# Optimization experiments

Hardware: AMD Instinct MI355X
Metric: run time of the kernel (lower is better)

## Reference

```python
import jax, jax.numpy as jnp
import numpy as np

B, T, S, D = 32, 1024, 1024, 512
VOCAB = 1000
INSERT_TOK = jnp.array([1, 2], dtype=jnp.int64)


def setup_inputs() -> dict:
    key = jax.random.key(0)
    k1, k2, k3, k4, k5 = jax.random.split(key, 5)
    input_var = jax.random.randint(k1, (B, T), 0, VOCAB, dtype=jnp.int64)
    output = jax.random.normal(k2, (B, T, D), jnp.float32)
    context = jax.random.normal(k3, (B, S, D), jnp.float32)
    # nn.Linear(2*dim, dim): weight [D, 2D], bias [D]
    W = jax.random.normal(k4, (D, 2 * D), jnp.float32) / np.sqrt(2 * D)
    b = jax.random.normal(k5, (D,), jnp.float32) * 0.01
    return {"input_var": input_var, "output": output, "context": context,
            "di": 0, "W": W, "b": b}


def _hard_align(input_var, src_len):
    """Replicates the python double-loop: sequential 'inserted' counter per batch.
    Returns (j, valid): j[b,i] = column of the 1.0 in attn row i (torch negative
    indices wrapped), valid[b,i] = whether row i gets any 1.0 at all."""
    bsz, tgt_len = input_var.shape
    flags = jnp.isin(input_var, INSERT_TOK)  # [B,T] is token an insert token

    def step(inserted, xi):
        i, flag = xi  # i: scalar position, flag: [B]
        cond = (src_len >= i - inserted)                    # gate, per batch
        ins2 = inserted + jnp.where(cond & flag, 1, 0)      # increment before write
        j = i - ins2 - 1
        j = jnp.where(j < 0, j + src_len, j)                # torch negative-index wrap
        return ins2, (j, cond)

    idxs = jnp.arange(1, tgt_len, dtype=jnp.int32)
    init = jnp.zeros((bsz,), jnp.int32)  # init_inserted()
    _, (j_rows, valid) = jax.lax.scan(step, init, (idxs, flags[:, 1:].T))
    j_rows = j_rows.T      # [B,T-1]
    valid = valid.T        # [B,T-1]
    # row 0: attn[b,0,0] = 1.0 always
    j_full = jnp.concatenate([jnp.zeros((bsz, 1), j_rows.dtype), j_rows], axis=1)
    valid_full = jnp.concatenate([jnp.ones((bsz, 1), bool), valid], axis=1)
    return j_full, valid_full


def reference(input_var, output, context, di, W, b):
    bsz, tgt_len, hid = output.shape
    src_len = context.shape[1]
    j, valid = _hard_align(input_var, src_len)              # [B,T], [B,T]
    vf = valid[:, :, None].astype(output.dtype)
    # hard one-hot attention matrix (as the module materializes it)
    attn = jax.nn.one_hot(j, src_len, dtype=output.dtype) * vf  # [B,T,S]
    # mix = bmm(attn, context) == masked gather of context rows
    mix = jnp.take_along_axis(context, j[:, :, None].astype(jnp.int32), axis=1) * vf
    combined = jnp.concatenate([mix, output], axis=-1)      # [B,T,2D]
    out = jnp.tanh(combined @ W.T + b)                      # [B,T,D]
    return out, attn
```

## Files before the change

### kernel.cpp

```cpp
#include <hip/hip_runtime.h>
#include <hip/hip_bf16.h>

#define B_ 32
#define T_ 1024
#define S_ 1024
#define D_ 512
#define M_ (B_*T_)
#define N_ D_
#define K_ (2*D_)

typedef __attribute__((ext_vector_type(8))) short bf16x8;
typedef __attribute__((ext_vector_type(4))) float f32x4;

__device__ inline unsigned short f2bf(float x) {
    union { float f; unsigned u; } v; v.f = x;
    unsigned r = v.u + 0x7FFFu + ((v.u >> 16) & 1u);
    return (unsigned short)(r >> 16);
}

__device__ inline unsigned cvt2bf(float lo, float hi) {
#if __has_builtin(__builtin_amdgcn_cvt_pk_bf16_f32)
    typedef __attribute__((ext_vector_type(2))) __bf16 bf2;
    union { bf2 v; unsigned u; } r;
    r.v = __builtin_amdgcn_cvt_pk_bf16_f32(lo, hi);
    return r.u;
#else
    return (unsigned)f2bf(lo) | ((unsigned)f2bf(hi) << 16);
#endif
}

__device__ inline float fast_tanh(float x) {
#if __has_builtin(__builtin_amdgcn_exp2f) && __has_builtin(__builtin_amdgcn_rcpf)
    const float e = __builtin_amdgcn_exp2f(x * 2.885390082f);
    const float r = __builtin_amdgcn_rcpf(e + 1.0f);
    return 1.0f - 2.0f * r;
#else
    return tanhf(x);
#endif
}

__global__ void align_kernel(const int* __restrict__ iv, int* __restrict__ jbuf) {
    const int b = blockIdx.x;
    const int lane = threadIdx.x;
    const int* row = iv + b * T_;
    int f[16];
    int local = 0;
    const int t0 = lane * 16;
    #pragma unroll
    for (int q = 0; q < 16; ++q) {
        const int t = t0 + q;
        const int tok = row[t];
        const int fl = (t > 0 && (tok == 1 || tok == 2)) ? 1 : 0;
        f[q] = fl;
        local += fl;
    }
    int incl = local;
    #pragma unroll
    for (int off = 1; off < 64; off <<= 1) {
        const int up = __shfl_up(incl, off, 64);
        if (lane >= off) incl += up;
    }
    int run = incl - local;
    #pragma unroll
    for (int q = 0; q < 16; ++q) {
        const int t = t0 + q;
        run += f[q];
        int j;
        if (t == 0) {
            j = 0;
        } else {
            j = t - run - 1;
            if (j < 0) j += S_;
        }
        jbuf[b * T_ + t] = j;
    }
}

__global__ void pack_w(const float* __restrict__ W, unsigned short* __restrict__ Wbf) {
    const int idx = blockIdx.x * blockDim.x + threadIdx.x;
    const f32x4 a = ((const f32x4*)W)[idx * 2];
    const f32x4 c = ((const f32x4*)W)[idx * 2 + 1];
    union { bf16x8 v; unsigned u[4]; } pk;
    pk.u[0] = cvt2bf(a[0], a[1]); pk.u[1] = cvt2bf(a[2], a[3]);
    pk.u[2] = cvt2bf(c[0], c[1]); pk.u[3] = cvt2bf(c[2], c[3]);
    *(bf16x8*)(Wbf + (size_t)idx * 8) = pk.v;
}

#define BM 256
#define BN 256
#define BK 64
#define NIT (K_ / BK)
#define KMAX (K_ - BK)
#define NGEMM ((M_ / BM) * (N_ / BN))

__global__ __launch_bounds__(512, 2)
void gemm_attn(const unsigned short* __restrict__ Wbf,
               const float* __restrict__ bias,
               float* __restrict__ out,
               float* __restrict__ attn,
               const float* __restrict__ ctx,
               const float* __restrict__ outp,
               const int* __restrict__ jbuf) {
    const int bx = blockIdx.x;
    const int tid = threadIdx.x;

    __shared__ unsigned short As[BM * BK];
    __shared__ unsigned short Bs[BN * BK];

    const int lane = tid & 63;
    const int wave = tid >> 6;
    const int wm = wave >> 1, wn = wave & 1;
    const int l16 = lane & 15, quad = lane >> 4;

    const int xcd = bx & 7;
    const int bn  = (bx >> 3) & 1;
    const int bm  = ((bx >> 4) << 3) | xcd;
    const int mBase = bm * BM;
    const int nBase = bn * BN;

    const int g    = tid & 7;
    const int rsub = tid >> 3;
    const int sw   = g ^ (rsub & 7);
    const float* actx[4];
    const float* aout[4];
    const unsigned short* bSrc[4];
    #pragma unroll
    for (int it = 0; it < 4; ++it) {
        const int r = it * 64 + rsub;
        const int m = mBase + r;
        const int jm = jbuf[m];
        actx[it] = ctx + ((size_t)((m >> 10) * S_ + jm)) * D_ + g * 8;
        aout[it] = outp + (size_t)m * D_ - D_ + g * 8;
        bSrc[it] = Wbf + (size_t)(nBase + r) * K_ + sw * 8;
    }

    const int aBase = mBase + bn * 128;

    f32x4 acc[4][8] = {};
    f32x4 fa[4][2];

#define LOAD_A(KO) do {                                                        \
    const int _koa = (KO);                                                     \
    _Pragma("unroll")                                                          \
    for (int _it = 0; _it < 4; ++_it) {                                        \
        const float* _src = (_koa < D_) ? (actx[_it] + _koa) : (aout[_it] + _koa); \
        fa[_it][0] = ((const f32x4*)_src)[0];                                  \
        fa[_it][1] = ((const f32x4*)_src)[1];                                  \
    }                                                                          \
} while (0)

    LOAD_A(0);

    #pragma unroll 1
    for (int i = 0; i < NIT; ++i) {
        const int ko = i * BK;
        #pragma unroll
        for (int it = 0; it < 4; ++it) {
            __builtin_amdgcn_global_load_lds(
                (const __attribute__((address_space(1))) void*)(bSrc[it] + ko),
                (__attribute__((address_space(3))) void*)(Bs + (it * 512 + tid) * 8),
                16, 0, 0);
        }
        #pragma unroll
        for (int it = 0; it < 4; ++it) {
            union { bf16x8 v; unsigned u[4]; } pk;
            pk.u[0] = cvt2bf(fa[it][0][0], fa[it][0][1]);
            pk.u[1] = cvt2bf(fa[it][0][2], fa[it][0][3]);
            pk.u[2] = cvt2bf(fa[it][1][0], fa[it][1][1]);
            pk.u[3] = cvt2bf(fa[it][1][2], fa[it][1][3]);
            *(bf16x8*)&As[(it * 512 + rsub * 8 + sw) * 8] = pk.v;
        }
        __syncthreads();

        {
            const int arow = aBase + i * 8 + wave;
            const int jv = jbuf[arow];
            f32x4* abase = (f32x4*)(attn + (size_t)arow * S_);
            #pragma unroll
            for (int s = 0; s < 4; ++s) {
                const int col = lane + 64 * s;
                f32x4 v = {0.f, 0.f, 0.f, 0.f};
                if ((jv >> 2) == col) v[jv & 3] = 1.0f;
                __builtin_nontemporal_store(v, abase + col);
            }
        }

        {
            const int ko2 = (ko + BK > KMAX) ? KMAX : ko + BK;
            LOAD_A(ko2);
        }

        #pragma unroll
        for (int ks = 0; ks < 2; ++ks) {
            bf16x8 af[4], bfr[8];
            const int q = ks * 4 + quad;
            #pragma unroll
            for (int mt = 0; mt < 4; ++mt) {
                const int r = wm * 64 + mt * 16 + l16;
                af[mt] = *(const bf16x8*)&As[(r * 8 + (q ^ (r & 7))) * 8];
            }
            #pragma unroll
            for (int nt = 0; nt < 8; ++nt) {
                const int rb = wn * 128 + nt * 16 + l16;
                bfr[nt] = *(const bf16x8*)&Bs[(rb * 8 + (q ^ (rb & 7))) * 8];
            }
            #pragma unroll
            for (int mt = 0; mt < 4; ++mt)
                #pragma unroll
                for (int nt = 0; nt < 8; ++nt)
                    acc[mt][nt] = __builtin_amdgcn_mfma_f32_16x16x32_bf16(
                        af[mt], bfr[nt], acc[mt][nt], 0, 0, 0);
        }
        __syncthreads();
    }

#undef LOAD_A

    #pragma unroll
    for (int nt = 0; nt < 8; ++nt) {
        const int n = nBase + wn * 128 + nt * 16 + l16;
        const float bv = bias[n];
        #pragma unroll
        for (int mt = 0; mt < 4; ++mt) {
            #pragma unroll
            for (int r = 0; r < 4; ++r) {
                const int m = mBase + wm * 64 + mt * 16 + quad * 4 + r;
                const float val = fast_tanh(acc[mt][nt][r] + bv);
                __builtin_nontemporal_store(val, &out[(size_t)m * N_ + n]);
            }
        }
    }
}

extern "C" void kernel_launch(void* const* d_in, const int* in_sizes, int n_in,
                              void* d_out, int out_size, void* d_ws, size_t ws_size,
                              hipStream_t stream) {
    const int*   iv   = (const int*)d_in[0];
    const float* outp = (const float*)d_in[1];
    const float* ctx  = (const float*)d_in[2];
    const float* W    = (const float*)d_in[4];
    const float* bias = (const float*)d_in[5];

    float* out  = (float*)d_out;
    float* attn = out + (size_t)M_ * N_;

    int* jbuf = (int*)d_ws;
    unsigned short* Wbf = (unsigned short*)((char*)d_ws + (size_t)M_ * 4);

    align_kernel<<<B_, 64, 0, stream>>>(iv, jbuf);
    pack_w<<<(N_ * K_ / 8) / 256, 256, 0, stream>>>(W, Wbf);
    gemm_attn<<<NGEMM, 512, 0, stream>>>(Wbf, bias, out, attn, ctx, outp, jbuf);
}
```

Baseline: 322.9 us.

## Double-buffer W tiles in LDS and fuse align and pack kernels

Splits the LDS buffer for the B (weight) tile into two halves. The DMA for the next K step is issued into the spare half right after the barrier, so it overlaps with the current step's MFMA work instead of being loaded at the top of each iteration. A scheduling barrier keeps the prefetch loads ahead of the compute. The align and weight-pack prologue kernels are merged into one launch to save a kernel launch. The larger LDS footprint (96KB per block) rules out two resident blocks per CU, although the grid is about one block per CU anyway.

```diff
diff --git a/kernel.cpp b/kernel.cpp
--- a/kernel.cpp
+++ b/kernel.cpp
@@ -39,45 +39,48 @@
 #endif
 }
 
-__global__ void align_kernel(const int* __restrict__ iv, int* __restrict__ jbuf) {
-    const int b = blockIdx.x;
-    const int lane = threadIdx.x;
-    const int* row = iv + b * T_;
-    int f[16];
-    int local = 0;
-    const int t0 = lane * 16;
-    #pragma unroll
-    for (int q = 0; q < 16; ++q) {
-        const int t = t0 + q;
-        const int tok = row[t];
-        const int fl = (t > 0 && (tok == 1 || tok == 2)) ? 1 : 0;
-        f[q] = fl;
-        local += fl;
-    }
-    int incl = local;
-    #pragma unroll
-    for (int off = 1; off < 64; off <<= 1) {
-        const int up = __shfl_up(incl, off, 64);
-        if (lane >= off) incl += up;
-    }
-    int run = incl - local;
-    #pragma unroll
-    for (int q = 0; q < 16; ++q) {
-        const int t = t0 + q;
-        run += f[q];
-        int j;
-        if (t == 0) {
-            j = 0;
-        } else {
-            j = t - run - 1;
-            if (j < 0) j += S_;
-        }
-        jbuf[b * T_ + t] = j;
-    }
-}
-
-__global__ void pack_w(const float* __restrict__ W, unsigned short* __restrict__ Wbf) {
-    const int idx = blockIdx.x * blockDim.x + threadIdx.x;
+__global__ __launch_bounds__(256)
+void align_pack(const int* __restrict__ iv, int* __restrict__ jbuf,
+                const float* __restrict__ W, unsigned short* __restrict__ Wbf) {
+    if (blockIdx.x < 32) {
+        if (threadIdx.x >= 64) return;
+        const int b = blockIdx.x;
+        const int lane = threadIdx.x;
+        const int* row = iv + b * T_;
+        int f[16];
+        int local = 0;
+        const int t0 = lane * 16;
+        #pragma unroll
+        for (int q = 0; q < 16; ++q) {
+            const int t = t0 + q;
+            const int tok = row[t];
+            const int fl = (t > 0 && (tok == 1 || tok == 2)) ? 1 : 0;
+            f[q] = fl;
+            local += fl;
+        }
+        int incl = local;
+        #pragma unroll
+        for (int off = 1; off < 64; off <<= 1) {
+            const int up = __shfl_up(incl, off, 64);
+            if (lane >= off) incl += up;
+        }
+        int run = incl - local;
+        #pragma unroll
+        for (int q = 0; q < 16; ++q) {
+            const int t = t0 + q;
+            run += f[q];
+            int j;
+            if (t == 0) {
+                j = 0;
+            } else {
+                j = t - run - 1;
+                if (j < 0) j += S_;
+            }
+            jbuf[b * T_ + t] = j;
+        }
+        return;
+    }
+    const int idx = (blockIdx.x - 32) * 256 + threadIdx.x;
     const f32x4 a = ((const f32x4*)W)[idx * 2];
     const f32x4 c = ((const f32x4*)W)[idx * 2 + 1];
     union { bf16x8 v; unsigned u[4]; } pk;
@@ -105,7 +108,7 @@
     const int tid = threadIdx.x;
 
     __shared__ unsigned short As[BM * BK];
-    __shared__ unsigned short Bs[BN * BK];
+    __shared__ unsigned short Bs[2][BN * BK];
 
     const int lane = tid & 63;
     const int wave = tid >> 6;
@@ -149,18 +152,26 @@
     }                                                                          \
 } while (0)
 
+#define DMA_B(P, KO) do {                                                      \
+    const int _kob = (KO);                                                     \
+    _Pragma("unroll")                                                          \
+    for (int _it = 0; _it < 4; ++_it) {                                        \
+        __builtin_amdgcn_global_load_lds(                                      \
+            (const __attribute__((address_space(1))) void*)(bSrc[_it] + _kob), \
+            (__attribute__((address_space(3))) void*)(&Bs[P][(_it * 512 + tid) * 8]), \
+            16, 0, 0);                                                         \
+    }                                                                          \
+} while (0)
+
     LOAD_A(0);
+    DMA_B(0, 0);
 
     #pragma unroll 1
     for (int i = 0; i < NIT; ++i) {
         const int ko = i * BK;
-        #pragma unroll
-        for (int it = 0; it < 4; ++it) {
-            __builtin_amdgcn_global_load_lds(
-                (const __attribute__((address_space(1))) void*)(bSrc[it] + ko),
-                (__attribute__((address_space(3))) void*)(Bs + (it * 512 + tid) * 8),
-                16, 0, 0);
-        }
+        const int p  = i & 1;
+        const int kon = (ko + BK > KMAX) ? KMAX : ko + BK;
+
         #pragma unroll
         for (int it = 0; it < 4; ++it) {
             union { bf16x8 v; unsigned u[4]; } pk;
@@ -184,11 +195,9 @@
                 __builtin_nontemporal_store(v, abase + col);
             }
         }
-
-        {
-            const int ko2 = (ko + BK > KMAX) ? KMAX : ko + BK;
-            LOAD_A(ko2);
-        }
+        LOAD_A(kon);
+        DMA_B(p ^ 1, kon);
+        __builtin_amdgcn_sched_barrier(0);
 
         #pragma unroll
         for (int ks = 0; ks < 2; ++ks) {
@@ -202,7 +211,7 @@
             #pragma unroll
             for (int nt = 0; nt < 8; ++nt) {
                 const int rb = wn * 128 + nt * 16 + l16;
-                bfr[nt] = *(const bf16x8*)&Bs[(rb * 8 + (q ^ (rb & 7))) * 8];
+                bfr[nt] = *(const bf16x8*)&Bs[p][(rb * 8 + (q ^ (rb & 7))) * 8];
             }
             #pragma unroll
             for (int mt = 0; mt < 4; ++mt)
@@ -215,6 +224,7 @@
     }
 
 #undef LOAD_A
+#undef DMA_B
 
     #pragma unroll
     for (int nt = 0; nt < 8; ++nt) {
@@ -247,7 +257,6 @@
     int* jbuf = (int*)d_ws;
     unsigned short* Wbf = (unsigned short*)((char*)d_ws + (size_t)M_ * 4);
 
-    align_kernel<<<B_, 64, 0, stream>>>(iv, jbuf);
-    pack_w<<<(N_ * K_ / 8) / 256, 256, 0, stream>>>(W, Wbf);
+    align_pack<<<32 + (N_ * K_ / 8) / 256, 256, 0, stream>>>(iv, jbuf, W, Wbf);
     gemm_attn<<<NGEMM, 512, 0, stream>>>(Wbf, bias, out, attn, ctx, outp, jbuf);
 }
```

Measured after the change: 323.5 us. About the same (+0.2%).
